# Performance work log

Hardware: AMD Instinct MI355X
Metric: run time of the kernel (lower is better)

The kernel has to match this reference:

```python
import jax, jax.numpy as jnp
import numpy as np

S = 4096  # sequence length (q_len == kv_len)
D = 1024  # feature dim


def setup_inputs() -> dict:
    key = jax.random.key(0)
    k1, k2, k3 = jax.random.split(key, 3)
    return {
        "query": jax.random.normal(k1, (1, S, D), dtype=jnp.float32),
        "key": jax.random.normal(k2, (1, S, D), dtype=jnp.float32),
        "value": jax.random.normal(k3, (S, D), dtype=jnp.float32),
    }


def reference(query, key, value):
    # key.transpose(1,2) then einsum('bij,bjk->bik') == contract over feature dim
    scores = jnp.einsum("bqd,bkd->bqk", query, key)  # [1, S, S] (NO 1/sqrt(d) scaling, faithful)
    attn = jax.nn.softmax(scores, axis=2)
    # torch.mm is a strict 2D matmul -> batch dim must be 1
    context = attn[0] @ value  # [S, D]
    return context
```

## Files before the change

### kernel.cpp

```cpp
#include <hip/hip_runtime.h>
#include <hip/hip_fp16.h>
#include <cstdint>
#include <cstddef>

typedef _Float16 f16;
typedef __attribute__((ext_vector_type(8))) _Float16 f16x8;
typedef __attribute__((ext_vector_type(4))) _Float16 f16x4;
typedef __attribute__((ext_vector_type(8))) short s16x8;
typedef __attribute__((ext_vector_type(4))) float f32x4;

#define S_LEN 4096
#define D_DIM 1024
#define SOFT_C 160.0f

template<int N> struct IC { static constexpr int v = N; };

__device__ __forceinline__ void gld_lds16(const void* g, void* l) {
    auto gp = reinterpret_cast<const unsigned int __attribute__((address_space(1)))*>(
        reinterpret_cast<uintptr_t>(g));
    auto lp = reinterpret_cast<unsigned int __attribute__((address_space(3)))*>(
        reinterpret_cast<uintptr_t>(l));
    __builtin_amdgcn_global_load_lds(gp, lp, 16, 0, 0);
}

template<int N> __device__ __forceinline__ void wait_vm() {
    if constexpr (N == 8)      asm volatile("s_waitcnt vmcnt(8)" ::: "memory");
    else if constexpr (N == 6) asm volatile("s_waitcnt vmcnt(6)" ::: "memory");
    else if constexpr (N == 4) asm volatile("s_waitcnt vmcnt(4)" ::: "memory");
    else if constexpr (N == 0) asm volatile("s_waitcnt vmcnt(0)" ::: "memory");
}

__device__ __forceinline__ unsigned short f2bf(float x) {
    unsigned u = __builtin_bit_cast(unsigned, x);
    u += 0x7FFFu + ((u >> 16) & 1u);
    return (unsigned short)(u >> 16);
}

__global__ __launch_bounds__(256)
void prep(const float* __restrict__ Q, const float* __restrict__ K,
          const float* __restrict__ V,
          f16* __restrict__ Qh, f16* __restrict__ Kh, unsigned short* __restrict__ Vt)
{
    const int b = blockIdx.x;
    if (b < 8192) {
        int idx = b * 256 + threadIdx.x;
        const int NQ4 = S_LEN * D_DIM / 4;
        const float* src;
        f16* dst;
        int i = idx;
        if (i < NQ4) { src = Q; dst = Qh; }
        else         { src = K; dst = Kh; i -= NQ4; }
        float4 v = ((const float4*)src)[i];
        f16x4 h = {(_Float16)v.x, (_Float16)v.y, (_Float16)v.z, (_Float16)v.w};
        *(f16x4*)&dst[(size_t)i * 4] = h;
    } else {
        __shared__ float tile[32][33];
        const int bb = b - 8192;
        const int bx = bb & 31;
        const int by = bb >> 5;
        const int tx = threadIdx.x & 31;
        const int ty = threadIdx.x >> 5;
#pragma unroll
        for (int j = 0; j < 4; ++j)
            tile[ty + j * 8][tx] = V[(size_t)(by * 32 + ty + j * 8) * D_DIM + bx * 32 + tx];
        __syncthreads();
#pragma unroll
        for (int j = 0; j < 4; ++j)
            Vt[(size_t)(bx * 32 + ty + j * 8) * S_LEN + by * 32 + tx] =
                f2bf(tile[tx][ty + j * 8]);
    }
}

__global__ __launch_bounds__(512, 2)
void gemm_exp(const f16* __restrict__ A, const f16* __restrict__ B,
              unsigned short* __restrict__ C, float* __restrict__ psum,
              int lda, int ldb, int ldc, int K, int tilesN)
{
    __shared__ f16 sA[4][256 * 32];
    __shared__ f16 sB[4][256 * 32];

    const int tid = threadIdx.x;
    const int w = tid >> 6;
    const int l = tid & 63;
    const int lr = l & 15;
    const int lk = l >> 4;
    const int wm = w >> 2;
    const int wn = w & 3;

    const int cpx = gridDim.x >> 3;
    const int bid = blockIdx.x;
    const int swz = (bid & 7) * cpx + (bid >> 3);
    const int tm = (swz / tilesN) * 256;
    const int tn = (swz % tilesN) * 256;
    const int NT = K >> 5;

    int offA[8], offB[4];
#pragma unroll
    for (int mi = 0; mi < 8; ++mi) {
        const int ra = wm * 128 + mi * 16 + lr;
        offA[mi] = ra * 32 + (lk ^ ((ra >> 1) & 3)) * 8;
    }
#pragma unroll
    for (int ni = 0; ni < 4; ++ni) {
        const int rb = wn * 64 + ni * 16 + lr;
        offB[ni] = rb * 32 + (lk ^ ((rb >> 1) & 3)) * 8;
    }

    auto stageA = [&](int rs, int t) {
        const int kt = t << 5;
#pragma unroll
        for (int r = 0; r < 2; ++r) {
            const int sbase = r * 512 + (w << 6);
            const int s = sbase + l;
            const int row = s >> 2;
            const int pos = s & 3;
            const int kb = pos ^ ((row >> 1) & 3);
            gld_lds16(A + (size_t)(tm + row) * lda + kt + kb * 8, &sA[rs][sbase * 8]);
        }
    };
    auto stageB = [&](int rs, int t) {
        const int kt = t << 5;
#pragma unroll
        for (int r = 0; r < 2; ++r) {
            const int sbase = r * 512 + (w << 6);
            const int s = sbase + l;
            const int row = s >> 2;
            const int pos = s & 3;
            const int kb = pos ^ ((row >> 1) & 3);
            gld_lds16(B + (size_t)(tn + row) * ldb + kt + kb * 8, &sB[rs][sbase * 8]);
        }
    };

    f32x4 acc[8][4] = {};
    f16x8 afA[4], bfA[4], afB[4], bfB[4];

    stageA(0, 0); stageB(0, 0);
    stageA(1, 1); stageB(1, 1);
    stageA(2, 2); stageB(2, 2);
    asm volatile("s_waitcnt vmcnt(8)" ::: "memory");
    __builtin_amdgcn_s_barrier();
    __builtin_amdgcn_sched_barrier(0);
#pragma unroll
    for (int i = 0; i < 4; ++i) afA[i] = *(const f16x8*)(&sA[0][0] + offA[i]);
#pragma unroll
    for (int i = 0; i < 4; ++i) bfA[i] = *(const f16x8*)(&sB[0][0] + offB[i]);

    auto tstep = [&](auto VMN, auto STG, auto LD1,
                     f16x8* af, f16x8* bf, f16x8* afn, f16x8* bfn, int t) {
        constexpr int vmn = decltype(VMN)::v;
        constexpr bool stg = decltype(STG)::v;
        constexpr bool ld1 = decltype(LD1)::v;
        const f16* sa = &sA[t & 3][0];

        __builtin_amdgcn_sched_barrier(0);
        f16x8 ag[4];
#pragma unroll
        for (int i = 0; i < 4; ++i) ag[i] = *(const f16x8*)(sa + offA[i + 4]);
        if constexpr (stg) stageA((t + 3) & 3, t + 3);
        __builtin_amdgcn_s_barrier();
        asm volatile("s_waitcnt lgkmcnt(4)" ::: "memory");
        __builtin_amdgcn_sched_barrier(0);
        __builtin_amdgcn_s_setprio(1);
#pragma unroll
        for (int mi = 0; mi < 4; ++mi)
#pragma unroll
            for (int ni = 0; ni < 4; ++ni)
                acc[mi][ni] = __builtin_amdgcn_mfma_f32_16x16x32_f16(
                    af[mi], bf[ni], acc[mi][ni], 0, 0, 0);
        __builtin_amdgcn_s_setprio(0);
        wait_vm<vmn>();
        __builtin_amdgcn_s_barrier();

        __builtin_amdgcn_sched_barrier(0);
        if constexpr (ld1) {
            const f16* na = &sA[(t + 1) & 3][0];
            const f16* nb = &sB[(t + 1) & 3][0];
#pragma unroll
            for (int i = 0; i < 4; ++i) afn[i] = *(const f16x8*)(na + offA[i]);
#pragma unroll
            for (int i = 0; i < 4; ++i) bfn[i] = *(const f16x8*)(nb + offB[i]);
        }
        if constexpr (stg) stageB((t + 3) & 3, t + 3);
        __builtin_amdgcn_s_barrier();
        if constexpr (ld1) asm volatile("s_waitcnt lgkmcnt(8)" ::: "memory");
        else               asm volatile("s_waitcnt lgkmcnt(0)" ::: "memory");
        __builtin_amdgcn_sched_barrier(0);
        __builtin_amdgcn_s_setprio(1);
#pragma unroll
        for (int mi = 0; mi < 4; ++mi)
#pragma unroll
            for (int ni = 0; ni < 4; ++ni)
                acc[mi + 4][ni] = __builtin_amdgcn_mfma_f32_16x16x32_f16(
                    ag[mi], bf[ni], acc[mi + 4][ni], 0, 0, 0);
        __builtin_amdgcn_s_setprio(0);
        __builtin_amdgcn_s_barrier();
    };

    for (int u = 0; u < NT / 2 - 2; ++u) {
        tstep(IC<6>{}, IC<true>{}, IC<true>{}, afA, bfA, afB, bfB, 2 * u);
        tstep(IC<6>{}, IC<true>{}, IC<true>{}, afB, bfB, afA, bfA, 2 * u + 1);
    }
    tstep(IC<6>{}, IC<true>{},  IC<true>{},  afA, bfA, afB, bfB, NT - 4);
    tstep(IC<4>{}, IC<false>{}, IC<true>{},  afB, bfB, afA, bfA, NT - 3);
    tstep(IC<0>{}, IC<false>{}, IC<true>{},  afA, bfA, afB, bfB, NT - 2);
    tstep(IC<0>{}, IC<false>{}, IC<false>{}, afB, bfB, afA, bfA, NT - 1);

    float rs[8][4];
#pragma unroll
    for (int mi = 0; mi < 8; ++mi)
#pragma unroll
        for (int j = 0; j < 4; ++j) rs[mi][j] = 0.f;

#pragma unroll
    for (int mi = 0; mi < 8; ++mi) {
        const int r0 = tm + wm * 128 + mi * 16 + (l >> 4) * 4;
#pragma unroll
        for (int ni = 0; ni < 4; ++ni) {
            const int c0 = tn + wn * 64 + ni * 16 + lr;
#pragma unroll
            for (int j = 0; j < 4; ++j) {
                float e = __expf(acc[mi][ni][j] - SOFT_C);
                C[(size_t)(r0 + j) * ldc + c0] = f2bf(e);
                rs[mi][j] += e;
            }
        }
    }
#pragma unroll
    for (int mi = 0; mi < 8; ++mi)
#pragma unroll
        for (int j = 0; j < 4; ++j)
#pragma unroll
            for (int m = 1; m < 16; m <<= 1)
                rs[mi][j] += __shfl_xor(rs[mi][j], m, 64);

    float* lsum = (float*)&sA[0][0];
    __syncthreads();
    if (lr == 0) {
#pragma unroll
        for (int mi = 0; mi < 8; ++mi)
#pragma unroll
            for (int j = 0; j < 4; ++j)
                lsum[wn * 256 + wm * 128 + mi * 16 + (l >> 4) * 4 + j] = rs[mi][j];
    }
    __syncthreads();
    if (tid < 256) {
        float s = (lsum[tid] + lsum[256 + tid]) + (lsum[512 + tid] + lsum[768 + tid]);
        psum[(size_t)(tn >> 8) * S_LEN + tm + tid] = s;
    }
}

__global__ __launch_bounds__(256)
void sumrows(const float* __restrict__ ps, float* __restrict__ invR)
{
    const int r = blockIdx.x * 256 + threadIdx.x;
    float s = 0.f;
#pragma unroll
    for (int j = 0; j < 16; ++j) s += ps[(size_t)j * S_LEN + r];
    invR[r] = 1.0f / s;
}

__global__ __launch_bounds__(512, 2)
void gemm_bt(const unsigned short* __restrict__ A, const unsigned short* __restrict__ B,
             unsigned short* __restrict__ P)
{
    __shared__ unsigned short sA[4][256 * 32];
    __shared__ unsigned short sB[4][256 * 32];

    const int tid = threadIdx.x;
    const int w = tid >> 6;
    const int l = tid & 63;
    const int lr = l & 15;
    const int lk = l >> 4;
    const int wm = w >> 2;
    const int wn = w & 3;

    const int cpx = gridDim.x >> 3;
    const int bid = blockIdx.x;
    const int swz = (bid & 7) * cpx + (bid >> 3);
    const int split = swz & 3;
    const int tidx = swz >> 2;
    const int tm = (tidx >> 2) * 256;
    const int tn = (tidx & 3) * 256;
    const int koff = split * 1024;
    unsigned short* Cp = P + (size_t)split * ((size_t)S_LEN * D_DIM);
    const int NT = 32;

    int offA[8], offB[4];
#pragma unroll
    for (int mi = 0; mi < 8; ++mi) {
        const int ra = wm * 128 + mi * 16 + lr;
        offA[mi] = ra * 32 + (lk ^ ((ra >> 1) & 3)) * 8;
    }
#pragma unroll
    for (int ni = 0; ni < 4; ++ni) {
        const int rb = wn * 64 + ni * 16 + lr;
        offB[ni] = rb * 32 + (lk ^ ((rb >> 1) & 3)) * 8;
    }

    auto stageA = [&](int rs, int t) {
        const int kt = koff + (t << 5);
#pragma unroll
        for (int r = 0; r < 2; ++r) {
            const int sbase = r * 512 + (w << 6);
            const int s = sbase + l;
            const int row = s >> 2;
            const int pos = s & 3;
            const int kb = pos ^ ((row >> 1) & 3);
            gld_lds16(A + (size_t)(tm + row) * S_LEN + kt + kb * 8, &sA[rs][sbase * 8]);
        }
    };
    auto stageB = [&](int rs, int t) {
        const int kt = koff + (t << 5);
#pragma unroll
        for (int r = 0; r < 2; ++r) {
            const int sbase = r * 512 + (w << 6);
            const int s = sbase + l;
            const int row = s >> 2;
            const int pos = s & 3;
            const int kb = pos ^ ((row >> 1) & 3);
            gld_lds16(B + (size_t)(tn + row) * S_LEN + kt + kb * 8, &sB[rs][sbase * 8]);
        }
    };

    f32x4 acc[8][4] = {};
    s16x8 afA[4], bfA[4], afB[4], bfB[4];

    stageA(0, 0); stageB(0, 0);
    stageA(1, 1); stageB(1, 1);
    stageA(2, 2); stageB(2, 2);
    asm volatile("s_waitcnt vmcnt(8)" ::: "memory");
    __builtin_amdgcn_s_barrier();
    __builtin_amdgcn_sched_barrier(0);
#pragma unroll
    for (int i = 0; i < 4; ++i) afA[i] = *(const s16x8*)(&sA[0][0] + offA[i]);
#pragma unroll
    for (int i = 0; i < 4; ++i) bfA[i] = *(const s16x8*)(&sB[0][0] + offB[i]);

    auto tstep = [&](auto VMN, auto STG, auto LD1,
                     s16x8* af, s16x8* bf, s16x8* afn, s16x8* bfn, int t) {
        constexpr int vmn = decltype(VMN)::v;
        constexpr bool stg = decltype(STG)::v;
        constexpr bool ld1 = decltype(LD1)::v;
        const unsigned short* sa = &sA[t & 3][0];

        __builtin_amdgcn_sched_barrier(0);
        s16x8 ag[4];
#pragma unroll
        for (int i = 0; i < 4; ++i) ag[i] = *(const s16x8*)(sa + offA[i + 4]);
        if constexpr (stg) stageA((t + 3) & 3, t + 3);
        __builtin_amdgcn_s_barrier();
        asm volatile("s_waitcnt lgkmcnt(4)" ::: "memory");
        __builtin_amdgcn_sched_barrier(0);
        __builtin_amdgcn_s_setprio(1);
#pragma unroll
        for (int mi = 0; mi < 4; ++mi)
#pragma unroll
            for (int ni = 0; ni < 4; ++ni)
                acc[mi][ni] = __builtin_amdgcn_mfma_f32_16x16x32_bf16(
                    af[mi], bf[ni], acc[mi][ni], 0, 0, 0);
        __builtin_amdgcn_s_setprio(0);
        wait_vm<vmn>();
        __builtin_amdgcn_s_barrier();

        __builtin_amdgcn_sched_barrier(0);
        if constexpr (ld1) {
            const unsigned short* na = &sA[(t + 1) & 3][0];
            const unsigned short* nb = &sB[(t + 1) & 3][0];
#pragma unroll
            for (int i = 0; i < 4; ++i) afn[i] = *(const s16x8*)(na + offA[i]);
#pragma unroll
            for (int i = 0; i < 4; ++i) bfn[i] = *(const s16x8*)(nb + offB[i]);
        }
        if constexpr (stg) stageB((t + 3) & 3, t + 3);
        __builtin_amdgcn_s_barrier();
        if constexpr (ld1) asm volatile("s_waitcnt lgkmcnt(8)" ::: "memory");
        else               asm volatile("s_waitcnt lgkmcnt(0)" ::: "memory");
        __builtin_amdgcn_sched_barrier(0);
        __builtin_amdgcn_s_setprio(1);
#pragma unroll
        for (int mi = 0; mi < 4; ++mi)
#pragma unroll
            for (int ni = 0; ni < 4; ++ni)
                acc[mi + 4][ni] = __builtin_amdgcn_mfma_f32_16x16x32_bf16(
                    ag[mi], bf[ni], acc[mi + 4][ni], 0, 0, 0);
        __builtin_amdgcn_s_setprio(0);
        __builtin_amdgcn_s_barrier();
    };

    for (int u = 0; u < NT / 2 - 2; ++u) {
        tstep(IC<6>{}, IC<true>{}, IC<true>{}, afA, bfA, afB, bfB, 2 * u);
        tstep(IC<6>{}, IC<true>{}, IC<true>{}, afB, bfB, afA, bfA, 2 * u + 1);
    }
    tstep(IC<6>{}, IC<true>{},  IC<true>{},  afA, bfA, afB, bfB, NT - 4);
    tstep(IC<4>{}, IC<false>{}, IC<true>{},  afB, bfB, afA, bfA, NT - 3);
    tstep(IC<0>{}, IC<false>{}, IC<true>{},  afA, bfA, afB, bfB, NT - 2);
    tstep(IC<0>{}, IC<false>{}, IC<false>{}, afB, bfB, afA, bfA, NT - 1);

#pragma unroll
    for (int mi = 0; mi < 8; ++mi) {
        const int r0 = tm + wm * 128 + mi * 16 + (l >> 4) * 4;
#pragma unroll
        for (int ni = 0; ni < 4; ++ni) {
            const int c0 = tn + wn * 64 + ni * 16 + lr;
#pragma unroll
            for (int j = 0; j < 4; ++j)
                Cp[(size_t)(r0 + j) * D_DIM + c0] = f2bf(acc[mi][ni][j]);
        }
    }
}

__global__ __launch_bounds__(256)
void combine4(const unsigned short* __restrict__ P, const float* __restrict__ invR,
              float* __restrict__ O)
{
    const size_t g = (size_t)blockIdx.x * 256 + threadIdx.x;
    const size_t n = (size_t)S_LEN * D_DIM;
    const int row = (int)(g >> 8);
    const float s = invR[row];
    float4 r = {0.f, 0.f, 0.f, 0.f};
#pragma unroll
    for (int sp = 0; sp < 4; ++sp) {
        uint2 u = ((const uint2*)(P + (size_t)sp * n))[g];
        r.x += __builtin_bit_cast(float, (u.x & 0xFFFFu) << 16);
        r.y += __builtin_bit_cast(float, u.x & 0xFFFF0000u);
        r.z += __builtin_bit_cast(float, (u.y & 0xFFFFu) << 16);
        r.w += __builtin_bit_cast(float, u.y & 0xFFFF0000u);
    }
    r.x *= s; r.y *= s; r.z *= s; r.w *= s;
    ((float4*)O)[g] = r;
}

__global__ __launch_bounds__(256)
void attn_naive(const float* __restrict__ Q, const float* __restrict__ K,
                const float* __restrict__ V, float* __restrict__ O)
{
    const int r = blockIdx.x;
    const int t = threadIdx.x;
    __shared__ float red[4];
    float q[4];
#pragma unroll
    for (int i = 0; i < 4; ++i) q[i] = Q[(size_t)r * D_DIM + t + i * 256];

    float m = -1e30f;
    for (int j = 0; j < S_LEN; ++j) {
        float p = 0.f;
#pragma unroll
        for (int i = 0; i < 4; ++i) p += q[i] * K[(size_t)j * D_DIM + t + i * 256];
#pragma unroll
        for (int off = 32; off > 0; off >>= 1) p += __shfl_xor(p, off, 64);
        if ((t & 63) == 0) red[t >> 6] = p;
        __syncthreads();
        float s = (red[0] + red[1]) + (red[2] + red[3]);
        __syncthreads();
        m = fmaxf(m, s);
    }
    float acc[4] = {0.f, 0.f, 0.f, 0.f};
    float lsum = 0.f;
    for (int j = 0; j < S_LEN; ++j) {
        float p = 0.f;
#pragma unroll
        for (int i = 0; i < 4; ++i) p += q[i] * K[(size_t)j * D_DIM + t + i * 256];
#pragma unroll
        for (int off = 32; off > 0; off >>= 1) p += __shfl_xor(p, off, 64);
        if ((t & 63) == 0) red[t >> 6] = p;
        __syncthreads();
        float s = (red[0] + red[1]) + (red[2] + red[3]);
        __syncthreads();
        float e = __expf(s - m);
        lsum += e;
#pragma unroll
        for (int i = 0; i < 4; ++i) acc[i] += e * V[(size_t)j * D_DIM + t + i * 256];
    }
    const float inv = 1.f / lsum;
#pragma unroll
    for (int i = 0; i < 4; ++i) O[(size_t)r * D_DIM + t + i * 256] = acc[i] * inv;
}

extern "C" void kernel_launch(void* const* d_in, const int* in_sizes, int n_in,
                              void* d_out, int out_size, void* d_ws, size_t ws_size,
                              hipStream_t stream)
{
    const float* Q = (const float*)d_in[0];
    const float* K = (const float*)d_in[1];
    const float* V = (const float*)d_in[2];
    float* O = (float*)d_out;

    const size_t MB = 1024ull * 1024ull;
    const size_t QH_OFF = 0;
    const size_t KH_OFF = 8 * MB;
    const size_t VT_OFF = 16 * MB;
    const size_t E_OFF  = 24 * MB;
    const size_t PS_OFF = 56 * MB;
    const size_t IV_OFF = 56 * MB + 512 * 1024;
    const size_t P_OFF  = 57 * MB;
    const size_t NEED   = 90 * MB;

    if (ws_size < NEED) {
        attn_naive<<<S_LEN, 256, 0, stream>>>(Q, K, V, O);
        return;
    }

    char* ws = (char*)d_ws;
    f16*            Qh  = (f16*)(ws + QH_OFF);
    f16*            Kh  = (f16*)(ws + KH_OFF);
    unsigned short* Vt  = (unsigned short*)(ws + VT_OFF);
    unsigned short* E   = (unsigned short*)(ws + E_OFF);
    float*          ps  = (float*)(ws + PS_OFF);
    float*          inv = (float*)(ws + IV_OFF);
    unsigned short* P   = (unsigned short*)(ws + P_OFF);

    prep<<<8192 + 4096, 256, 0, stream>>>(Q, K, V, Qh, Kh, Vt);

    gemm_exp<<<256, 512, 0, stream>>>(Qh, Kh, E, ps, D_DIM, D_DIM, S_LEN,
                                      D_DIM, 16);

    sumrows<<<16, 256, 0, stream>>>(ps, inv);

    gemm_bt<<<256, 512, 0, stream>>>(E, Vt, P);

    combine4<<<S_LEN * D_DIM / 4 / 256, 256, 0, stream>>>(P, inv, O);
}
```

Measured before the change: 99.08 us.

## Restructure both GEMM main loops into 64-wide k-steps with two-stage prefetch

Replaces the templated 3-deep prefetch pipeline (register double-buffered fragments, partial lgkmcnt waits) in both the QK and PV GEMM kernels with a loop that processes two 32-wide k-slices per iteration. Each iteration has four phases that load fragments, issue the next global-to-LDS stage and run half the MFMAs. It prefetches only two slices ahead and waits with lgkmcnt(0) before each MFMA batch. This simplifies scheduling and frees the second set of fragment registers, but it reduces the prefetch depth and adds more barriers and full LDS waits, so memory latency may be less well hidden.

After: 100.0 us. About the same (+0.9%).

```diff
diff --git a/kernel.cpp b/kernel.cpp
--- a/kernel.cpp
+++ b/kernel.cpp
@@ -12,8 +12,6 @@
 #define S_LEN 4096
 #define D_DIM 1024
 #define SOFT_C 160.0f
-
-template<int N> struct IC { static constexpr int v = N; };
 
 __device__ __forceinline__ void gld_lds16(const void* g, void* l) {
     auto gp = reinterpret_cast<const unsigned int __attribute__((address_space(1)))*>(
@@ -23,18 +21,16 @@
     __builtin_amdgcn_global_load_lds(gp, lp, 16, 0, 0);
 }
 
-template<int N> __device__ __forceinline__ void wait_vm() {
-    if constexpr (N == 8)      asm volatile("s_waitcnt vmcnt(8)" ::: "memory");
-    else if constexpr (N == 6) asm volatile("s_waitcnt vmcnt(6)" ::: "memory");
-    else if constexpr (N == 4) asm volatile("s_waitcnt vmcnt(4)" ::: "memory");
-    else if constexpr (N == 0) asm volatile("s_waitcnt vmcnt(0)" ::: "memory");
-}
-
 __device__ __forceinline__ unsigned short f2bf(float x) {
     unsigned u = __builtin_bit_cast(unsigned, x);
     u += 0x7FFFu + ((u >> 16) & 1u);
     return (unsigned short)(u >> 16);
 }
+
+#define SCHED0() __builtin_amdgcn_sched_barrier(0)
+#define BAR()    __builtin_amdgcn_s_barrier()
+#define LGKM0()  asm volatile("s_waitcnt lgkmcnt(0)" ::: "memory")
+#define VM(n)    asm volatile("s_waitcnt vmcnt(" #n ")" ::: "memory")
 
 __global__ __launch_bounds__(256)
 void prep(const float* __restrict__ Q, const float* __restrict__ K,
@@ -92,7 +88,7 @@
     const int swz = (bid & 7) * cpx + (bid >> 3);
     const int tm = (swz / tilesN) * 256;
     const int tn = (swz % tilesN) * 256;
-    const int NT = K >> 5;
+    const int NT = K >> 6;
 
     int offA[8], offB[4];
 #pragma unroll
@@ -106,8 +102,7 @@
         offB[ni] = rb * 32 + (lk ^ ((rb >> 1) & 3)) * 8;
     }
 
-    auto stageA = [&](int rs, int t) {
-        const int kt = t << 5;
+    auto stA = [&](int slot, int gk) {
 #pragma unroll
         for (int r = 0; r < 2; ++r) {
             const int sbase = r * 512 + (w << 6);
@@ -115,11 +110,10 @@
             const int row = s >> 2;
             const int pos = s & 3;
             const int kb = pos ^ ((row >> 1) & 3);
-            gld_lds16(A + (size_t)(tm + row) * lda + kt + kb * 8, &sA[rs][sbase * 8]);
+            gld_lds16(A + (size_t)(tm + row) * lda + gk + kb * 8, &sA[slot][sbase * 8]);
         }
     };
-    auto stageB = [&](int rs, int t) {
-        const int kt = t << 5;
+    auto stB = [&](int slot, int gk) {
 #pragma unroll
         for (int r = 0; r < 2; ++r) {
             const int sbase = r * 512 + (w << 6);
@@ -127,83 +121,103 @@
             const int row = s >> 2;
             const int pos = s & 3;
             const int kb = pos ^ ((row >> 1) & 3);
-            gld_lds16(B + (size_t)(tn + row) * ldb + kt + kb * 8, &sB[rs][sbase * 8]);
+            gld_lds16(B + (size_t)(tn + row) * ldb + gk + kb * 8, &sB[slot][sbase * 8]);
         }
     };
 
     f32x4 acc[8][4] = {};
-    f16x8 afA[4], bfA[4], afB[4], bfB[4];
-
-    stageA(0, 0); stageB(0, 0);
-    stageA(1, 1); stageB(1, 1);
-    stageA(2, 2); stageB(2, 2);
-    asm volatile("s_waitcnt vmcnt(8)" ::: "memory");
-    __builtin_amdgcn_s_barrier();
-    __builtin_amdgcn_sched_barrier(0);
-#pragma unroll
-    for (int i = 0; i < 4; ++i) afA[i] = *(const f16x8*)(&sA[0][0] + offA[i]);
-#pragma unroll
-    for (int i = 0; i < 4; ++i) bfA[i] = *(const f16x8*)(&sB[0][0] + offB[i]);
-
-    auto tstep = [&](auto VMN, auto STG, auto LD1,
-                     f16x8* af, f16x8* bf, f16x8* afn, f16x8* bfn, int t) {
-        constexpr int vmn = decltype(VMN)::v;
-        constexpr bool stg = decltype(STG)::v;
-        constexpr bool ld1 = decltype(LD1)::v;
-        const f16* sa = &sA[t & 3][0];
-
-        __builtin_amdgcn_sched_barrier(0);
-        f16x8 ag[4];
-#pragma unroll
-        for (int i = 0; i < 4; ++i) ag[i] = *(const f16x8*)(sa + offA[i + 4]);
-        if constexpr (stg) stageA((t + 3) & 3, t + 3);
-        __builtin_amdgcn_s_barrier();
-        asm volatile("s_waitcnt lgkmcnt(4)" ::: "memory");
-        __builtin_amdgcn_sched_barrier(0);
-        __builtin_amdgcn_s_setprio(1);
-#pragma unroll
-        for (int mi = 0; mi < 4; ++mi)
-#pragma unroll
-            for (int ni = 0; ni < 4; ++ni)
-                acc[mi][ni] = __builtin_amdgcn_mfma_f32_16x16x32_f16(
-                    af[mi], bf[ni], acc[mi][ni], 0, 0, 0);
-        __builtin_amdgcn_s_setprio(0);
-        wait_vm<vmn>();
-        __builtin_amdgcn_s_barrier();
-
-        __builtin_amdgcn_sched_barrier(0);
-        if constexpr (ld1) {
-            const f16* na = &sA[(t + 1) & 3][0];
-            const f16* nb = &sB[(t + 1) & 3][0];
-#pragma unroll
-            for (int i = 0; i < 4; ++i) afn[i] = *(const f16x8*)(na + offA[i]);
-#pragma unroll
-            for (int i = 0; i < 4; ++i) bfn[i] = *(const f16x8*)(nb + offB[i]);
-        }
-        if constexpr (stg) stageB((t + 3) & 3, t + 3);
-        __builtin_amdgcn_s_barrier();
-        if constexpr (ld1) asm volatile("s_waitcnt lgkmcnt(8)" ::: "memory");
-        else               asm volatile("s_waitcnt lgkmcnt(0)" ::: "memory");
-        __builtin_amdgcn_sched_barrier(0);
-        __builtin_amdgcn_s_setprio(1);
-#pragma unroll
-        for (int mi = 0; mi < 4; ++mi)
-#pragma unroll
-            for (int ni = 0; ni < 4; ++ni)
-                acc[mi + 4][ni] = __builtin_amdgcn_mfma_f32_16x16x32_f16(
-                    ag[mi], bf[ni], acc[mi + 4][ni], 0, 0, 0);
-        __builtin_amdgcn_s_setprio(0);
-        __builtin_amdgcn_s_barrier();
-    };
-
-    for (int u = 0; u < NT / 2 - 2; ++u) {
-        tstep(IC<6>{}, IC<true>{}, IC<true>{}, afA, bfA, afB, bfB, 2 * u);
-        tstep(IC<6>{}, IC<true>{}, IC<true>{}, afB, bfB, afA, bfA, 2 * u + 1);
-    }
-    tstep(IC<6>{}, IC<true>{},  IC<true>{},  afA, bfA, afB, bfB, NT - 4);
-    tstep(IC<4>{}, IC<false>{}, IC<true>{},  afB, bfB, afA, bfA, NT - 3);
-    tstep(IC<0>{}, IC<false>{}, IC<true>{},  afA, bfA, afB, bfB, NT - 2);
-    tstep(IC<0>{}, IC<false>{}, IC<false>{}, afB, bfB, afA, bfA, NT - 1);
+    f16x8 af[4], bf[4];
+
+#define MFMA_HALF(base)                                                        \
+    __builtin_amdgcn_s_setprio(1);                                             \
+    _Pragma("unroll")                                                          \
+    for (int mi = 0; mi < 4; ++mi)                                             \
+        _Pragma("unroll")                                                      \
+        for (int ni = 0; ni < 4; ++ni)                                         \
+            acc[(base) + mi][ni] = __builtin_amdgcn_mfma_f32_16x16x32_f16(     \
+                af[mi], bf[ni], acc[(base) + mi][ni], 0, 0, 0);                \
+    __builtin_amdgcn_s_setprio(0);
+
+    stA(0, 0); stB(0, 0);
+    stA(1, 32); stB(1, 32);
+    VM(4);
+    BAR();
+
+    for (int t = 0; t < NT - 1; ++t) {
+        const int sa0 = (2 * t) & 3, sa1 = (2 * t + 1) & 3;
+        const int na0 = (2 * t + 2) & 3, na1 = (2 * t + 3) & 3;
+        const int nk = (t + 1) << 6;
+
+        SCHED0();
+#pragma unroll
+        for (int i = 0; i < 4; ++i) af[i] = *(const f16x8*)(&sA[sa0][0] + offA[i]);
+#pragma unroll
+        for (int i = 0; i < 4; ++i) bf[i] = *(const f16x8*)(&sB[sa0][0] + offB[i]);
+        stA(na0, nk);
+        BAR(); LGKM0(); SCHED0();
+        MFMA_HALF(0)
+        VM(4); BAR();
+
+        SCHED0();
+#pragma unroll
+        for (int i = 0; i < 4; ++i) af[i] = *(const f16x8*)(&sA[sa0][0] + offA[4 + i]);
+        stB(na0, nk);
+        BAR(); LGKM0(); SCHED0();
+        MFMA_HALF(4)
+        VM(4); BAR();
+
+        SCHED0();
+#pragma unroll
+        for (int i = 0; i < 4; ++i) af[i] = *(const f16x8*)(&sA[sa1][0] + offA[i]);
+#pragma unroll
+        for (int i = 0; i < 4; ++i) bf[i] = *(const f16x8*)(&sB[sa1][0] + offB[i]);
+        stA(na1, nk + 32);
+        BAR(); LGKM0(); SCHED0();
+        MFMA_HALF(0)
+        VM(4); BAR();
+
+        SCHED0();
+#pragma unroll
+        for (int i = 0; i < 4; ++i) af[i] = *(const f16x8*)(&sA[sa1][0] + offA[4 + i]);
+        stB(na1, nk + 32);
+        BAR(); LGKM0(); SCHED0();
+        MFMA_HALF(4)
+        VM(4); BAR();
+    }
+    {
+        const int sa0 = (2 * (NT - 1)) & 3, sa1 = (2 * (NT - 1) + 1) & 3;
+        SCHED0();
+#pragma unroll
+        for (int i = 0; i < 4; ++i) af[i] = *(const f16x8*)(&sA[sa0][0] + offA[i]);
+#pragma unroll
+        for (int i = 0; i < 4; ++i) bf[i] = *(const f16x8*)(&sB[sa0][0] + offB[i]);
+        BAR(); LGKM0(); SCHED0();
+        MFMA_HALF(0)
+        VM(2); BAR();
+
+        SCHED0();
+#pragma unroll
+        for (int i = 0; i < 4; ++i) af[i] = *(const f16x8*)(&sA[sa0][0] + offA[4 + i]);
+        BAR(); LGKM0(); SCHED0();
+        MFMA_HALF(4)
+        VM(0); BAR();
+
+        SCHED0();
+#pragma unroll
+        for (int i = 0; i < 4; ++i) af[i] = *(const f16x8*)(&sA[sa1][0] + offA[i]);
+#pragma unroll
+        for (int i = 0; i < 4; ++i) bf[i] = *(const f16x8*)(&sB[sa1][0] + offB[i]);
+        BAR(); LGKM0(); SCHED0();
+        MFMA_HALF(0)
+        BAR();
+
+        SCHED0();
+#pragma unroll
+        for (int i = 0; i < 4; ++i) af[i] = *(const f16x8*)(&sA[sa1][0] + offA[4 + i]);
+        BAR(); LGKM0(); SCHED0();
+        MFMA_HALF(4)
+    }
+#undef MFMA_HALF
 
     float rs[8][4];
 #pragma unroll
@@ -283,7 +297,7 @@
     const int tn = (tidx & 3) * 256;
     const int koff = split * 1024;
     unsigned short* Cp = P + (size_t)split * ((size_t)S_LEN * D_DIM);
-    const int NT = 32;
+    const int NT = 16;
 
     int offA[8], offB[4];
 #pragma unroll
@@ -297,8 +311,7 @@
         offB[ni] = rb * 32 + (lk ^ ((rb >> 1) & 3)) * 8;
     }
 
-    auto stageA = [&](int rs, int t) {
-        const int kt = koff + (t << 5);
+    auto stA = [&](int slot, int gk) {
 #pragma unroll
         for (int r = 0; r < 2; ++r) {
             const int sbase = r * 512 + (w << 6);
@@ -306,11 +319,10 @@
             const int row = s >> 2;
             const int pos = s & 3;
             const int kb = pos ^ ((row >> 1) & 3);
-            gld_lds16(A + (size_t)(tm + row) * S_LEN + kt + kb * 8, &sA[rs][sbase * 8]);
+            gld_lds16(A + (size_t)(tm + row) * S_LEN + gk + kb * 8, &sA[slot][sbase * 8]);
         }
     };
-    auto stageB = [&](int rs, int t) {
-        const int kt = koff + (t << 5);
+    auto stB = [&](int slot, int gk) {
 #pragma unroll
         for (int r = 0; r < 2; ++r) {
             const int sbase = r * 512 + (w << 6);
@@ -318,83 +330,103 @@
             const int row = s >> 2;
             const int pos = s & 3;
             const int kb = pos ^ ((row >> 1) & 3);
-            gld_lds16(B + (size_t)(tn + row) * S_LEN + kt + kb * 8, &sB[rs][sbase * 8]);
+            gld_lds16(B + (size_t)(tn + row) * S_LEN + gk + kb * 8, &sB[slot][sbase * 8]);
         }
     };
 
     f32x4 acc[8][4] = {};
-    s16x8 afA[4], bfA[4], afB[4], bfB[4];
-
-    stageA(0, 0); stageB(0, 0);
-    stageA(1, 1); stageB(1, 1);
-    stageA(2, 2); stageB(2, 2);
-    asm volatile("s_waitcnt vmcnt(8)" ::: "memory");
-    __builtin_amdgcn_s_barrier();
-    __builtin_amdgcn_sched_barrier(0);
-#pragma unroll
-    for (int i = 0; i < 4; ++i) afA[i] = *(const s16x8*)(&sA[0][0] + offA[i]);
-#pragma unroll
-    for (int i = 0; i < 4; ++i) bfA[i] = *(const s16x8*)(&sB[0][0] + offB[i]);
-
-    auto tstep = [&](auto VMN, auto STG, auto LD1,
-                     s16x8* af, s16x8* bf, s16x8* afn, s16x8* bfn, int t) {
-        constexpr int vmn = decltype(VMN)::v;
-        constexpr bool stg = decltype(STG)::v;
-        constexpr bool ld1 = decltype(LD1)::v;
-        const unsigned short* sa = &sA[t & 3][0];
-
-        __builtin_amdgcn_sched_barrier(0);
-        s16x8 ag[4];
-#pragma unroll
-        for (int i = 0; i < 4; ++i) ag[i] = *(const s16x8*)(sa + offA[i + 4]);
-        if constexpr (stg) stageA((t + 3) & 3, t + 3);
-        __builtin_amdgcn_s_barrier();
-        asm volatile("s_waitcnt lgkmcnt(4)" ::: "memory");
-        __builtin_amdgcn_sched_barrier(0);
-        __builtin_amdgcn_s_setprio(1);
-#pragma unroll
-        for (int mi = 0; mi < 4; ++mi)
-#pragma unroll
-            for (int ni = 0; ni < 4; ++ni)
-                acc[mi][ni] = __builtin_amdgcn_mfma_f32_16x16x32_bf16(
-                    af[mi], bf[ni], acc[mi][ni], 0, 0, 0);
-        __builtin_amdgcn_s_setprio(0);
-        wait_vm<vmn>();
-        __builtin_amdgcn_s_barrier();
-
-        __builtin_amdgcn_sched_barrier(0);
-        if constexpr (ld1) {
-            const unsigned short* na = &sA[(t + 1) & 3][0];
-            const unsigned short* nb = &sB[(t + 1) & 3][0];
-#pragma unroll
-            for (int i = 0; i < 4; ++i) afn[i] = *(const s16x8*)(na + offA[i]);
-#pragma unroll
-            for (int i = 0; i < 4; ++i) bfn[i] = *(const s16x8*)(nb + offB[i]);
-        }
-        if constexpr (stg) stageB((t + 3) & 3, t + 3);
-        __builtin_amdgcn_s_barrier();
-        if constexpr (ld1) asm volatile("s_waitcnt lgkmcnt(8)" ::: "memory");
-        else               asm volatile("s_waitcnt lgkmcnt(0)" ::: "memory");
-        __builtin_amdgcn_sched_barrier(0);
-        __builtin_amdgcn_s_setprio(1);
-#pragma unroll
-        for (int mi = 0; mi < 4; ++mi)
-#pragma unroll
-            for (int ni = 0; ni < 4; ++ni)
-                acc[mi + 4][ni] = __builtin_amdgcn_mfma_f32_16x16x32_bf16(
-                    ag[mi], bf[ni], acc[mi + 4][ni], 0, 0, 0);
-        __builtin_amdgcn_s_setprio(0);
-        __builtin_amdgcn_s_barrier();
-    };
-
-    for (int u = 0; u < NT / 2 - 2; ++u) {
-        tstep(IC<6>{}, IC<true>{}, IC<true>{}, afA, bfA, afB, bfB, 2 * u);
-        tstep(IC<6>{}, IC<true>{}, IC<true>{}, afB, bfB, afA, bfA, 2 * u + 1);
-    }
-    tstep(IC<6>{}, IC<true>{},  IC<true>{},  afA, bfA, afB, bfB, NT - 4);
-    tstep(IC<4>{}, IC<false>{}, IC<true>{},  afB, bfB, afA, bfA, NT - 3);
-    tstep(IC<0>{}, IC<false>{}, IC<true>{},  afA, bfA, afB, bfB, NT - 2);
-    tstep(IC<0>{}, IC<false>{}, IC<false>{}, afB, bfB, afA, bfA, NT - 1);
+    s16x8 af[4], bf[4];
+
+#define MFMA_HALF(base)                                                        \
+    __builtin_amdgcn_s_setprio(1);                                             \
+    _Pragma("unroll")                                                          \
+    for (int mi = 0; mi < 4; ++mi)                                             \
+        _Pragma("unroll")                                                      \
+        for (int ni = 0; ni < 4; ++ni)                                         \
+            acc[(base) + mi][ni] = __builtin_amdgcn_mfma_f32_16x16x32_bf16(    \
+                af[mi], bf[ni], acc[(base) + mi][ni], 0, 0, 0);                \
+    __builtin_amdgcn_s_setprio(0);
+
+    stA(0, koff); stB(0, koff);
+    stA(1, koff + 32); stB(1, koff + 32);
+    VM(4);
+    BAR();
+
+    for (int t = 0; t < NT - 1; ++t) {
+        const int sa0 = (2 * t) & 3, sa1 = (2 * t + 1) & 3;
+        const int na0 = (2 * t + 2) & 3, na1 = (2 * t + 3) & 3;
+        const int nk = koff + ((t + 1) << 6);
+
+        SCHED0();
+#pragma unroll
+        for (int i = 0; i < 4; ++i) af[i] = *(const s16x8*)(&sA[sa0][0] + offA[i]);
+#pragma unroll
+        for (int i = 0; i < 4; ++i) bf[i] = *(const s16x8*)(&sB[sa0][0] + offB[i]);
+        stA(na0, nk);
+        BAR(); LGKM0(); SCHED0();
+        MFMA_HALF(0)
+        VM(4); BAR();
+
+        SCHED0();
+#pragma unroll
+        for (int i = 0; i < 4; ++i) af[i] = *(const s16x8*)(&sA[sa0][0] + offA[4 + i]);
+        stB(na0, nk);
+        BAR(); LGKM0(); SCHED0();
+        MFMA_HALF(4)
+        VM(4); BAR();
+
+        SCHED0();
+#pragma unroll
+        for (int i = 0; i < 4; ++i) af[i] = *(const s16x8*)(&sA[sa1][0] + offA[i]);
+#pragma unroll
+        for (int i = 0; i < 4; ++i) bf[i] = *(const s16x8*)(&sB[sa1][0] + offB[i]);
+        stA(na1, nk + 32);
+        BAR(); LGKM0(); SCHED0();
+        MFMA_HALF(0)
+        VM(4); BAR();
+
+        SCHED0();
+#pragma unroll
+        for (int i = 0; i < 4; ++i) af[i] = *(const s16x8*)(&sA[sa1][0] + offA[4 + i]);
+        stB(na1, nk + 32);
+        BAR(); LGKM0(); SCHED0();
+        MFMA_HALF(4)
+        VM(4); BAR();
+    }
+    {
+        const int sa0 = (2 * (NT - 1)) & 3, sa1 = (2 * (NT - 1) + 1) & 3;
+        SCHED0();
+#pragma unroll
+        for (int i = 0; i < 4; ++i) af[i] = *(const s16x8*)(&sA[sa0][0] + offA[i]);
+#pragma unroll
+        for (int i = 0; i < 4; ++i) bf[i] = *(const s16x8*)(&sB[sa0][0] + offB[i]);
+        BAR(); LGKM0(); SCHED0();
+        MFMA_HALF(0)
+        VM(2); BAR();
+
+        SCHED0();
+#pragma unroll
+        for (int i = 0; i < 4; ++i) af[i] = *(const s16x8*)(&sA[sa0][0] + offA[4 + i]);
+        BAR(); LGKM0(); SCHED0();
+        MFMA_HALF(4)
+        VM(0); BAR();
+
+        SCHED0();
+#pragma unroll
+        for (int i = 0; i < 4; ++i) af[i] = *(const s16x8*)(&sA[sa1][0] + offA[i]);
+#pragma unroll
+        for (int i = 0; i < 4; ++i) bf[i] = *(const s16x8*)(&sB[sa1][0] + offB[i]);
+        BAR(); LGKM0(); SCHED0();
+        MFMA_HALF(0)
+        BAR();
+
+        SCHED0();
+#pragma unroll
+        for (int i = 0; i < 4; ++i) af[i] = *(const s16x8*)(&sA[sa1][0] + offA[4 + i]);
+        BAR(); LGKM0(); SCHED0();
+        MFMA_HALF(4)
+    }
+#undef MFMA_HALF
 
 #pragma unroll
     for (int mi = 0; mi < 8; ++mi) {
```

## Restructure GEMM main loops to process two K-slices per iteration with double-buffered stages

Applied to the files above, without the earlier changes.

Both GEMM kernels (QK^T scores and PV) now handle 64 K-elements per loop iteration by loading two 32-wide LDS slots at once and issuing twice as many MFMAs between barriers. The old template-unrolled tstep pipeline, with its register ping-pong prefetch and 3-deep staging, becomes a plain loop with 2-deep staging in pairs of slots and full lgkmcnt(0) waits. The aim is to halve the barrier and wait count per unit of work. In exchange it drops the cross-step register prefetch, so LDS read latency is less hidden, and it uses more fragment registers.

Result: faster. 95.99 us (-3.1%).

```diff
diff --git a/kernel.cpp b/kernel.cpp
--- a/kernel.cpp
+++ b/kernel.cpp
@@ -12,8 +12,6 @@
 #define S_LEN 4096
 #define D_DIM 1024
 #define SOFT_C 160.0f
-
-template<int N> struct IC { static constexpr int v = N; };
 
 __device__ __forceinline__ void gld_lds16(const void* g, void* l) {
     auto gp = reinterpret_cast<const unsigned int __attribute__((address_space(1)))*>(
@@ -23,18 +21,16 @@
     __builtin_amdgcn_global_load_lds(gp, lp, 16, 0, 0);
 }
 
-template<int N> __device__ __forceinline__ void wait_vm() {
-    if constexpr (N == 8)      asm volatile("s_waitcnt vmcnt(8)" ::: "memory");
-    else if constexpr (N == 6) asm volatile("s_waitcnt vmcnt(6)" ::: "memory");
-    else if constexpr (N == 4) asm volatile("s_waitcnt vmcnt(4)" ::: "memory");
-    else if constexpr (N == 0) asm volatile("s_waitcnt vmcnt(0)" ::: "memory");
-}
-
 __device__ __forceinline__ unsigned short f2bf(float x) {
     unsigned u = __builtin_bit_cast(unsigned, x);
     u += 0x7FFFu + ((u >> 16) & 1u);
     return (unsigned short)(u >> 16);
 }
+
+#define SCHED0() __builtin_amdgcn_sched_barrier(0)
+#define BAR()    __builtin_amdgcn_s_barrier()
+#define LGKM0()  asm volatile("s_waitcnt lgkmcnt(0)" ::: "memory")
+#define VM(n)    asm volatile("s_waitcnt vmcnt(" #n ")" ::: "memory")
 
 __global__ __launch_bounds__(256)
 void prep(const float* __restrict__ Q, const float* __restrict__ K,
@@ -92,7 +88,7 @@
     const int swz = (bid & 7) * cpx + (bid >> 3);
     const int tm = (swz / tilesN) * 256;
     const int tn = (swz % tilesN) * 256;
-    const int NT = K >> 5;
+    const int NT = K >> 6;
 
     int offA[8], offB[4];
 #pragma unroll
@@ -106,104 +102,94 @@
         offB[ni] = rb * 32 + (lk ^ ((rb >> 1) & 3)) * 8;
     }
 
-    auto stageA = [&](int rs, int t) {
-        const int kt = t << 5;
-#pragma unroll
-        for (int r = 0; r < 2; ++r) {
-            const int sbase = r * 512 + (w << 6);
-            const int s = sbase + l;
-            const int row = s >> 2;
-            const int pos = s & 3;
-            const int kb = pos ^ ((row >> 1) & 3);
-            gld_lds16(A + (size_t)(tm + row) * lda + kt + kb * 8, &sA[rs][sbase * 8]);
+    auto stA2 = [&](int t) {
+        const int gk = t << 6;
+#pragma unroll
+        for (int kh = 0; kh < 2; ++kh) {
+            const int slot = (2 * t + kh) & 3;
+#pragma unroll
+            for (int r = 0; r < 2; ++r) {
+                const int sbase = r * 512 + (w << 6);
+                const int s = sbase + l;
+                const int row = s >> 2;
+                const int pos = s & 3;
+                const int kb = pos ^ ((row >> 1) & 3);
+                gld_lds16(A + (size_t)(tm + row) * lda + gk + kh * 32 + kb * 8,
+                          &sA[slot][sbase * 8]);
+            }
         }
     };
-    auto stageB = [&](int rs, int t) {
-        const int kt = t << 5;
-#pragma unroll
-        for (int r = 0; r < 2; ++r) {
-            const int sbase = r * 512 + (w << 6);
-            const int s = sbase + l;
-            const int row = s >> 2;
-            const int pos = s & 3;
-            const int kb = pos ^ ((row >> 1) & 3);
-            gld_lds16(B + (size_t)(tn + row) * ldb + kt + kb * 8, &sB[rs][sbase * 8]);
+    auto stB2 = [&](int t) {
+        const int gk = t << 6;
+#pragma unroll
+        for (int kh = 0; kh < 2; ++kh) {
+            const int slot = (2 * t + kh) & 3;
+#pragma unroll
+            for (int r = 0; r < 2; ++r) {
+                const int sbase = r * 512 + (w << 6);
+                const int s = sbase + l;
+                const int row = s >> 2;
+                const int pos = s & 3;
+                const int kb = pos ^ ((row >> 1) & 3);
+                gld_lds16(B + (size_t)(tn + row) * ldb + gk + kh * 32 + kb * 8,
+                          &sB[slot][sbase * 8]);
+            }
         }
     };
 
     f32x4 acc[8][4] = {};
-    f16x8 afA[4], bfA[4], afB[4], bfB[4];
-
-    stageA(0, 0); stageB(0, 0);
-    stageA(1, 1); stageB(1, 1);
-    stageA(2, 2); stageB(2, 2);
-    asm volatile("s_waitcnt vmcnt(8)" ::: "memory");
-    __builtin_amdgcn_s_barrier();
-    __builtin_amdgcn_sched_barrier(0);
-#pragma unroll
-    for (int i = 0; i < 4; ++i) afA[i] = *(const f16x8*)(&sA[0][0] + offA[i]);
-#pragma unroll
-    for (int i = 0; i < 4; ++i) bfA[i] = *(const f16x8*)(&sB[0][0] + offB[i]);
-
-    auto tstep = [&](auto VMN, auto STG, auto LD1,
-                     f16x8* af, f16x8* bf, f16x8* afn, f16x8* bfn, int t) {
-        constexpr int vmn = decltype(VMN)::v;
-        constexpr bool stg = decltype(STG)::v;
-        constexpr bool ld1 = decltype(LD1)::v;
-        const f16* sa = &sA[t & 3][0];
-
-        __builtin_amdgcn_sched_barrier(0);
-        f16x8 ag[4];
-#pragma unroll
-        for (int i = 0; i < 4; ++i) ag[i] = *(const f16x8*)(sa + offA[i + 4]);
-        if constexpr (stg) stageA((t + 3) & 3, t + 3);
-        __builtin_amdgcn_s_barrier();
-        asm volatile("s_waitcnt lgkmcnt(4)" ::: "memory");
-        __builtin_amdgcn_sched_barrier(0);
+    f16x8 af[2][4], bf[2][4], ag[2][4];
+
+    stA2(0); stB2(0);
+    stA2(1); stB2(1);
+    VM(8);
+    BAR();
+
+    for (int t = 0; t < NT; ++t) {
+        const int s0 = (2 * t) & 3, s1 = (2 * t + 1) & 3;
+
+        SCHED0();
+#pragma unroll
+        for (int i = 0; i < 4; ++i) af[0][i] = *(const f16x8*)(&sA[s0][0] + offA[i]);
+#pragma unroll
+        for (int i = 0; i < 4; ++i) af[1][i] = *(const f16x8*)(&sA[s1][0] + offA[i]);
+#pragma unroll
+        for (int i = 0; i < 4; ++i) bf[0][i] = *(const f16x8*)(&sB[s0][0] + offB[i]);
+#pragma unroll
+        for (int i = 0; i < 4; ++i) bf[1][i] = *(const f16x8*)(&sB[s1][0] + offB[i]);
+        BAR(); LGKM0(); SCHED0();
+        if (t + 2 < NT) stB2(t + 2);
         __builtin_amdgcn_s_setprio(1);
 #pragma unroll
-        for (int mi = 0; mi < 4; ++mi)
-#pragma unroll
-            for (int ni = 0; ni < 4; ++ni)
-                acc[mi][ni] = __builtin_amdgcn_mfma_f32_16x16x32_f16(
-                    af[mi], bf[ni], acc[mi][ni], 0, 0, 0);
+        for (int kh = 0; kh < 2; ++kh)
+#pragma unroll
+            for (int mi = 0; mi < 4; ++mi)
+#pragma unroll
+                for (int ni = 0; ni < 4; ++ni)
+                    acc[mi][ni] = __builtin_amdgcn_mfma_f32_16x16x32_f16(
+                        af[kh][mi], bf[kh][ni], acc[mi][ni], 0, 0, 0);
         __builtin_amdgcn_s_setprio(0);
-        wait_vm<vmn>();
-        __builtin_amdgcn_s_barrier();
-
-        __builtin_amdgcn_sched_barrier(0);
-        if constexpr (ld1) {
-            const f16* na = &sA[(t + 1) & 3][0];
-            const f16* nb = &sB[(t + 1) & 3][0];
-#pragma unroll
-            for (int i = 0; i < 4; ++i) afn[i] = *(const f16x8*)(na + offA[i]);
-#pragma unroll
-            for (int i = 0; i < 4; ++i) bfn[i] = *(const f16x8*)(nb + offB[i]);
-        }
-        if constexpr (stg) stageB((t + 3) & 3, t + 3);
-        __builtin_amdgcn_s_barrier();
-        if constexpr (ld1) asm volatile("s_waitcnt lgkmcnt(8)" ::: "memory");
-        else               asm volatile("s_waitcnt lgkmcnt(0)" ::: "memory");
-        __builtin_amdgcn_sched_barrier(0);
+
+        SCHED0();
+#pragma unroll
+        for (int i = 0; i < 4; ++i) ag[0][i] = *(const f16x8*)(&sA[s0][0] + offA[4 + i]);
+#pragma unroll
+        for (int i = 0; i < 4; ++i) ag[1][i] = *(const f16x8*)(&sA[s1][0] + offA[4 + i]);
+        if (t + 2 < NT)      { VM(4); }
+        else if (t + 1 < NT) { VM(0); }
+        BAR(); LGKM0(); SCHED0();
+        if (t + 2 < NT) stA2(t + 2);
         __builtin_amdgcn_s_setprio(1);
 #pragma unroll
-        for (int mi = 0; mi < 4; ++mi)
-#pragma unroll
-            for (int ni = 0; ni < 4; ++ni)
-                acc[mi + 4][ni] = __builtin_amdgcn_mfma_f32_16x16x32_f16(
-                    ag[mi], bf[ni], acc[mi + 4][ni], 0, 0, 0);
+        for (int kh = 0; kh < 2; ++kh)
+#pragma unroll
+            for (int mi = 0; mi < 4; ++mi)
+#pragma unroll
+                for (int ni = 0; ni < 4; ++ni)
+                    acc[4 + mi][ni] = __builtin_amdgcn_mfma_f32_16x16x32_f16(
+                        ag[kh][mi], bf[kh][ni], acc[4 + mi][ni], 0, 0, 0);
         __builtin_amdgcn_s_setprio(0);
-        __builtin_amdgcn_s_barrier();
-    };
-
-    for (int u = 0; u < NT / 2 - 2; ++u) {
-        tstep(IC<6>{}, IC<true>{}, IC<true>{}, afA, bfA, afB, bfB, 2 * u);
-        tstep(IC<6>{}, IC<true>{}, IC<true>{}, afB, bfB, afA, bfA, 2 * u + 1);
-    }
-    tstep(IC<6>{}, IC<true>{},  IC<true>{},  afA, bfA, afB, bfB, NT - 4);
-    tstep(IC<4>{}, IC<false>{}, IC<true>{},  afB, bfB, afA, bfA, NT - 3);
-    tstep(IC<0>{}, IC<false>{}, IC<true>{},  afA, bfA, afB, bfB, NT - 2);
-    tstep(IC<0>{}, IC<false>{}, IC<false>{}, afB, bfB, afA, bfA, NT - 1);
+    }
 
     float rs[8][4];
 #pragma unroll
@@ -283,7 +269,7 @@
     const int tn = (tidx & 3) * 256;
     const int koff = split * 1024;
     unsigned short* Cp = P + (size_t)split * ((size_t)S_LEN * D_DIM);
-    const int NT = 32;
+    const int NT = 16;
 
     int offA[8], offB[4];
 #pragma unroll
@@ -297,104 +283,94 @@
         offB[ni] = rb * 32 + (lk ^ ((rb >> 1) & 3)) * 8;
     }
 
-    auto stageA = [&](int rs, int t) {
-        const int kt = koff + (t << 5);
-#pragma unroll
-        for (int r = 0; r < 2; ++r) {
-            const int sbase = r * 512 + (w << 6);
-            const int s = sbase + l;
-            const int row = s >> 2;
-            const int pos = s & 3;
-            const int kb = pos ^ ((row >> 1) & 3);
-            gld_lds16(A + (size_t)(tm + row) * S_LEN + kt + kb * 8, &sA[rs][sbase * 8]);
+    auto stA2 = [&](int t) {
+        const int gk = koff + (t << 6);
+#pragma unroll
+        for (int kh = 0; kh < 2; ++kh) {
+            const int slot = (2 * t + kh) & 3;
+#pragma unroll
+            for (int r = 0; r < 2; ++r) {
+                const int sbase = r * 512 + (w << 6);
+                const int s = sbase + l;
+                const int row = s >> 2;
+                const int pos = s & 3;
+                const int kb = pos ^ ((row >> 1) & 3);
+                gld_lds16(A + (size_t)(tm + row) * S_LEN + gk + kh * 32 + kb * 8,
+                          &sA[slot][sbase * 8]);
+            }
         }
     };
-    auto stageB = [&](int rs, int t) {
-        const int kt = koff + (t << 5);
-#pragma unroll
-        for (int r = 0; r < 2; ++r) {
-            const int sbase = r * 512 + (w << 6);
-            const int s = sbase + l;
-            const int row = s >> 2;
-            const int pos = s & 3;
-            const int kb = pos ^ ((row >> 1) & 3);
-            gld_lds16(B + (size_t)(tn + row) * S_LEN + kt + kb * 8, &sB[rs][sbase * 8]);
+    auto stB2 = [&](int t) {
+        const int gk = koff + (t << 6);
+#pragma unroll
+        for (int kh = 0; kh < 2; ++kh) {
+            const int slot = (2 * t + kh) & 3;
+#pragma unroll
+            for (int r = 0; r < 2; ++r) {
+                const int sbase = r * 512 + (w << 6);
+                const int s = sbase + l;
+                const int row = s >> 2;
+                const int pos = s & 3;
+                const int kb = pos ^ ((row >> 1) & 3);
+                gld_lds16(B + (size_t)(tn + row) * S_LEN + gk + kh * 32 + kb * 8,
+                          &sB[slot][sbase * 8]);
+            }
         }
     };
 
     f32x4 acc[8][4] = {};
-    s16x8 afA[4], bfA[4], afB[4], bfB[4];
-
-    stageA(0, 0); stageB(0, 0);
-    stageA(1, 1); stageB(1, 1);
-    stageA(2, 2); stageB(2, 2);
-    asm volatile("s_waitcnt vmcnt(8)" ::: "memory");
-    __builtin_amdgcn_s_barrier();
-    __builtin_amdgcn_sched_barrier(0);
-#pragma unroll
-    for (int i = 0; i < 4; ++i) afA[i] = *(const s16x8*)(&sA[0][0] + offA[i]);
-#pragma unroll
-    for (int i = 0; i < 4; ++i) bfA[i] = *(const s16x8*)(&sB[0][0] + offB[i]);
-
-    auto tstep = [&](auto VMN, auto STG, auto LD1,
-                     s16x8* af, s16x8* bf, s16x8* afn, s16x8* bfn, int t) {
-        constexpr int vmn = decltype(VMN)::v;
-        constexpr bool stg = decltype(STG)::v;
-        constexpr bool ld1 = decltype(LD1)::v;
-        const unsigned short* sa = &sA[t & 3][0];
-
-        __builtin_amdgcn_sched_barrier(0);
-        s16x8 ag[4];
-#pragma unroll
-        for (int i = 0; i < 4; ++i) ag[i] = *(const s16x8*)(sa + offA[i + 4]);
-        if constexpr (stg) stageA((t + 3) & 3, t + 3);
-        __builtin_amdgcn_s_barrier();
-        asm volatile("s_waitcnt lgkmcnt(4)" ::: "memory");
-        __builtin_amdgcn_sched_barrier(0);
+    s16x8 af[2][4], bf[2][4], ag[2][4];
+
+    stA2(0); stB2(0);
+    stA2(1); stB2(1);
+    VM(8);
+    BAR();
+
+    for (int t = 0; t < NT; ++t) {
+        const int s0 = (2 * t) & 3, s1 = (2 * t + 1) & 3;
+
+        SCHED0();
+#pragma unroll
+        for (int i = 0; i < 4; ++i) af[0][i] = *(const s16x8*)(&sA[s0][0] + offA[i]);
+#pragma unroll
+        for (int i = 0; i < 4; ++i) af[1][i] = *(const s16x8*)(&sA[s1][0] + offA[i]);
+#pragma unroll
+        for (int i = 0; i < 4; ++i) bf[0][i] = *(const s16x8*)(&sB[s0][0] + offB[i]);
+#pragma unroll
+        for (int i = 0; i < 4; ++i) bf[1][i] = *(const s16x8*)(&sB[s1][0] + offB[i]);
+        BAR(); LGKM0(); SCHED0();
+        if (t + 2 < NT) stB2(t + 2);
         __builtin_amdgcn_s_setprio(1);
 #pragma unroll
-        for (int mi = 0; mi < 4; ++mi)
-#pragma unroll
-            for (int ni = 0; ni < 4; ++ni)
-                acc[mi][ni] = __builtin_amdgcn_mfma_f32_16x16x32_bf16(
-                    af[mi], bf[ni], acc[mi][ni], 0, 0, 0);
+        for (int kh = 0; kh < 2; ++kh)
+#pragma unroll
+            for (int mi = 0; mi < 4; ++mi)
+#pragma unroll
+                for (int ni = 0; ni < 4; ++ni)
+                    acc[mi][ni] = __builtin_amdgcn_mfma_f32_16x16x32_bf16(
+                        af[kh][mi], bf[kh][ni], acc[mi][ni], 0, 0, 0);
         __builtin_amdgcn_s_setprio(0);
-        wait_vm<vmn>();
-        __builtin_amdgcn_s_barrier();
-
-        __builtin_amdgcn_sched_barrier(0);
-        if constexpr (ld1) {
-            const unsigned short* na = &sA[(t + 1) & 3][0];
-            const unsigned short* nb = &sB[(t + 1) & 3][0];
-#pragma unroll
-            for (int i = 0; i < 4; ++i) afn[i] = *(const s16x8*)(na + offA[i]);
-#pragma unroll
-            for (int i = 0; i < 4; ++i) bfn[i] = *(const s16x8*)(nb + offB[i]);
-        }
-        if constexpr (stg) stageB((t + 3) & 3, t + 3);
-        __builtin_amdgcn_s_barrier();
-        if constexpr (ld1) asm volatile("s_waitcnt lgkmcnt(8)" ::: "memory");
-        else               asm volatile("s_waitcnt lgkmcnt(0)" ::: "memory");
-        __builtin_amdgcn_sched_barrier(0);
+
+        SCHED0();
+#pragma unroll
+        for (int i = 0; i < 4; ++i) ag[0][i] = *(const s16x8*)(&sA[s0][0] + offA[4 + i]);
+#pragma unroll
+        for (int i = 0; i < 4; ++i) ag[1][i] = *(const s16x8*)(&sA[s1][0] + offA[4 + i]);
+        if (t + 2 < NT)      { VM(4); }
+        else if (t + 1 < NT) { VM(0); }
+        BAR(); LGKM0(); SCHED0();
+        if (t + 2 < NT) stA2(t + 2);
         __builtin_amdgcn_s_setprio(1);
 #pragma unroll
-        for (int mi = 0; mi < 4; ++mi)
-#pragma unroll
-            for (int ni = 0; ni < 4; ++ni)
-                acc[mi + 4][ni] = __builtin_amdgcn_mfma_f32_16x16x32_bf16(
-                    ag[mi], bf[ni], acc[mi + 4][ni], 0, 0, 0);
+        for (int kh = 0; kh < 2; ++kh)
+#pragma unroll
+            for (int mi = 0; mi < 4; ++mi)
+#pragma unroll
+                for (int ni = 0; ni < 4; ++ni)
+                    acc[4 + mi][ni] = __builtin_amdgcn_mfma_f32_16x16x32_bf16(
+                        ag[kh][mi], bf[kh][ni], acc[4 + mi][ni], 0, 0, 0);
         __builtin_amdgcn_s_setprio(0);
-        __builtin_amdgcn_s_barrier();
-    };
-
-    for (int u = 0; u < NT / 2 - 2; ++u) {
-        tstep(IC<6>{}, IC<true>{}, IC<true>{}, afA, bfA, afB, bfB, 2 * u);
-        tstep(IC<6>{}, IC<true>{}, IC<true>{}, afB, bfB, afA, bfA, 2 * u + 1);
-    }
-    tstep(IC<6>{}, IC<true>{},  IC<true>{},  afA, bfA, afB, bfB, NT - 4);
-    tstep(IC<4>{}, IC<false>{}, IC<true>{},  afB, bfB, afA, bfA, NT - 3);
-    tstep(IC<0>{}, IC<false>{}, IC<true>{},  afA, bfA, afB, bfB, NT - 2);
-    tstep(IC<0>{}, IC<false>{}, IC<false>{}, afB, bfB, afA, bfA, NT - 1);
+    }
 
 #pragma unroll
     for (int mi = 0; mi < 8; ++mi) {
```
